# Kernel tuning notes

Measured on AMD Instinct MI355X. Metric: run time of the kernel, lower is better.

Reference implementation:

```python
import jax, jax.numpy as jnp
import numpy as np

T, H, W_, CIN, LAT, HID, OUT, NHL = 32, 64, 64, 3, 256, 256, 3, 3
OMEGA = 30.0  # SIREN sine frequency


def _uniform(key, shape, fan_in):
    b = np.sqrt(6.0 / fan_in) / OMEGA
    return jax.random.uniform(key, shape, jnp.float32, -b, b)


def setup_inputs() -> dict:
    key = jax.random.key(0)
    ks = jax.random.split(key, 10)
    return {
        "coords": jax.random.normal(ks[0], (T, H, W_, CIN), jnp.float32),
        "latents": jax.random.normal(ks[1], (T, LAT), jnp.float32),
        # shared SIREN weights (nf_net): W stored as (out, in) like nn.Linear
        "W0": _uniform(ks[2], (HID, CIN), CIN),
        "b0": jnp.zeros((HID,), jnp.float32),
        "Wh": _uniform(ks[3], (NHL, HID, HID), HID),
        "bh": jnp.zeros((NHL, HID), jnp.float32),
        "Wf": _uniform(ks[4], (OUT, HID), HID),
        "bf": jnp.zeros((OUT,), jnp.float32),
        # hypernet weight generators (hw_net), no bias
        "HW0": _uniform(ks[5], (HID * CIN, LAT), LAT),
        "HWh": _uniform(ks[6], (NHL, HID * HID, LAT), LAT),
        # hypernet bias generators (hb_net), no bias
        "HB": _uniform(ks[7], (NHL + 1, HID, LAT), LAT),
    }


def reference(coords, latents, W0, b0, Wh, bh, Wf, bf, HW0, HWh, HB):
    t = latents.shape[0]
    # per-frame hyper biases for all layers: (t, NHL+1, HID)
    hb = jnp.einsum('tl,khl->tkh', latents, HB)
    # layer 0: per-frame weight (t, HID, CIN)
    hw0 = (latents @ HW0.T).reshape(t, HID, CIN)
    x = coords  # (t,h,w,CIN)
    x = (x @ W0.T + b0
         + jnp.einsum('thwi,toi->thwo', x, hw0)
         + hb[:, 0][:, None, None, :])
    x = jnp.sin(OMEGA * x)
    for i in range(NHL):
        hw = (latents @ HWh[i].T).reshape(t, HID, HID)  # (t, HID, HID)
        x = (x @ Wh[i].T + bh[i]
             + jnp.einsum('thwi,toi->thwo', x, hw)
             + hb[:, i + 1][:, None, None, :])
        x = jnp.sin(OMEGA * x)
    return x @ Wf.T + bf  # (t,h,w,OUT)
```

## Files before the change

### kernel.cpp

```cpp
#include <hip/hip_runtime.h>
#include <cstdint>
#include <cstddef>

typedef __attribute__((ext_vector_type(8))) _Float16 f16x8;
typedef __attribute__((ext_vector_type(16))) float f32x16;

#define LO_SCALE 2048.0f
#define LO_INV   (1.0f / 2048.0f)

union H8 { f16x8 v; _Float16 h[8]; };

__global__ __launch_bounds__(256) void kab(
    const float* __restrict__ latents, const float* __restrict__ W0,
    const float* __restrict__ b0, const float* __restrict__ bh,
    const float* __restrict__ HW0, const float* __restrict__ HB,
    const float* __restrict__ Wh, const float* __restrict__ HWh,
    _Float16* __restrict__ w0blob, float* __restrict__ beff,
    _Float16* __restrict__ whblob) {
  __shared__ float lat_t[8192];
  int tid = threadIdx.x, bid = blockIdx.x;

  if (bid >= 768) {
    int id = (bid - 768) * 256 + tid;
    if (id < 32768) {
      int t = id >> 10, rem = id & 1023;
      int r2 = rem & 127, part = r2 >> 6, lane = r2 & 63;
      int nf = rem >> 7;
      int o = nf * 32 + (lane & 31), kc = lane >> 5;
      const float* lat = latents + t * 256;
      H8 outv;
#pragma unroll
      for (int j = 0; j < 8; ++j) outv.h[j] = (_Float16)0.0f;
#pragma unroll
      for (int j = 0; j < 8; ++j) {
        int i = kc * 8 + j;
        if (i < 3) {
          const float* row = HW0 + (o * 3 + i) * 256;
          float s = W0[o * 3 + i];
          for (int k = 0; k < 256; k += 4)
            s += row[k] * lat[k] + row[k + 1] * lat[k + 1] +
                 row[k + 2] * lat[k + 2] + row[k + 3] * lat[k + 3];
          _Float16 hi = (_Float16)s;
          outv.h[j] = part ? (_Float16)((s - (float)hi) * LO_SCALE) : hi;
        }
      }
      *(f16x8*)(w0blob + (size_t)id * 8) = outv.v;
    } else {
      int v = id - 32768;
      int t = v >> 10, k = (v >> 8) & 3, hm = v & 255;
      float base = (k == 0) ? b0[hm] : bh[(k - 1) * 256 + hm];
      const float* lat = latents + t * 256;
      const float* row = HB + (size_t)(k * 256 + hm) * 256;
      float s = base;
      for (int kk = 0; kk < 256; kk += 4)
        s += row[kk] * lat[kk] + row[kk + 1] * lat[kk + 1] +
             row[kk + 2] * lat[kk + 2] + row[kk + 3] * lat[kk + 3];
      beff[v] = s;
    }
    return;
  }

  int h = bid & 1, ks = (bid >> 1) & 15, nf = (bid >> 5) & 7, l = bid >> 8;

  {
    int f = tid >> 3, kb = (tid & 7) * 32;
#pragma unroll
    for (int m = 0; m < 32; m += 4) {
      float4 v = *(const float4*)(latents + f * 256 + kb + m);
      lat_t[(kb + m + 0) * 32 + f] = v.x;
      lat_t[(kb + m + 1) * 32 + f] = v.y;
      lat_t[(kb + m + 2) * 32 + f] = v.z;
      lat_t[(kb + m + 3) * 32 + f] = v.w;
    }
  }
  __syncthreads();

  int oo = tid >> 3, jj = tid & 7;
  int o = nf * 32 + oo;
  int i = ks * 16 + h * 8 + jj;
  int r = o * 256 + i;
  const float* rowp = HWh + ((size_t)l * 65536 + (size_t)r) * 256;

  float acc[32];
#pragma unroll
  for (int f = 0; f < 32; ++f) acc[f] = 0.f;

  float curf[16], nxtf[16];
#pragma unroll
  for (int q = 0; q < 4; ++q)
    *(float4*)(curf + q * 4) = *(const float4*)(rowp + q * 4);

  for (int kc = 0; kc < 16; ++kc) {
    if (kc < 15) {
#pragma unroll
      for (int q = 0; q < 4; ++q)
        *(float4*)(nxtf + q * 4) = *(const float4*)(rowp + (kc + 1) * 16 + q * 4);
    }
    const float* lp = lat_t + kc * 512;
#pragma unroll
    for (int m = 0; m < 16; ++m) {
      float hw = curf[m];
#pragma unroll
      for (int fq = 0; fq < 8; ++fq) {
        float4 lv = *(const float4*)(lp + m * 32 + fq * 4);
        acc[fq * 4 + 0] += hw * lv.x;
        acc[fq * 4 + 1] += hw * lv.y;
        acc[fq * 4 + 2] += hw * lv.z;
        acc[fq * 4 + 3] += hw * lv.w;
      }
    }
#pragma unroll
    for (int q = 0; q < 16; ++q) curf[q] = nxtf[q];
  }

  float whv = Wh[l * 65536 + r];
  size_t cbase = (size_t)(nf * 16 + ks) * 1024 + (size_t)h * 256 + (size_t)tid;
#pragma unroll
  for (int t = 0; t < 32; ++t) {
    float w = acc[t] + whv;
    _Float16 hi = (_Float16)w;
    _Float16 lo = (_Float16)((w - (float)hi) * LO_SCALE);
    size_t b = (size_t)(t * 3 + l) * 131072 + cbase;
    whblob[b] = hi;
    whblob[b + 512] = lo;
  }
}

__global__ __launch_bounds__(512, 6) void kb_siren(
    const float* __restrict__ coords, const _Float16* __restrict__ whblob,
    const _Float16* __restrict__ w0blob, const float* __restrict__ beff,
    const float* __restrict__ Wf, const float* __restrict__ bf,
    float* __restrict__ out) {
  __shared__ _Float16 xs_hi[32 * 264];
  __shared__ _Float16 xs_lo[32 * 264];
  __shared__ float wf_s[768];
  __shared__ float red[768];
  int tid = threadIdx.x;
  int bid0 = blockIdx.x;
  int bid = (bid0 & 7) * 512 + (bid0 >> 3);
  int t = bid >> 7, tile = bid & 127;
  int wv = tid >> 6, lane = tid & 63, col = lane & 31, h = lane >> 5;

  if (tid < 192) *(float4*)(wf_s + tid * 4) = *(const float4*)(Wf + tid * 4);
  if (tid < 32) {
    const float* cp = coords + (size_t)(t * 4096 + tile * 32 + tid) * 3;
    float c0 = cp[0], c1 = cp[1], c2 = cp[2];
    H8 hv, lv, z;
#pragma unroll
    for (int j = 0; j < 8; ++j) { hv.h[j] = (_Float16)0.f; lv.h[j] = (_Float16)0.f; z.h[j] = (_Float16)0.f; }
    _Float16 h0 = (_Float16)c0, h1 = (_Float16)c1, h2 = (_Float16)c2;
    hv.h[0] = h0; hv.h[1] = h1; hv.h[2] = h2;
    lv.h[0] = (_Float16)((c0 - (float)h0) * LO_SCALE);
    lv.h[1] = (_Float16)((c1 - (float)h1) * LO_SCALE);
    lv.h[2] = (_Float16)((c2 - (float)h2) * LO_SCALE);
    *(f16x8*)(xs_hi + tid * 264) = hv.v;
    *(f16x8*)(xs_lo + tid * 264) = lv.v;
    *(f16x8*)(xs_hi + tid * 264 + 8) = z.v;
    *(f16x8*)(xs_lo + tid * 264 + 8) = z.v;
  }
  __syncthreads();

  f32x16 accA, accB;

  auto init_bias = [&](int bk) {
    const float* bp = beff + ((t * 4 + bk) << 8) + wv * 32 + h * 4;
#pragma unroll
    for (int rq = 0; rq < 4; ++rq) {
      float4 bvv = *(const float4*)(bp + rq * 8);
      float ba[4];
      *(float4*)ba = bvv;
#pragma unroll
      for (int q = 0; q < 4; ++q) {
        accA[rq * 4 + q] = ba[q];
        accB[rq * 4 + q] = 0.f;
      }
    }
  };

  auto load_a = [&](const _Float16* blobL, int NS, int ks, f16x8 (&a)[2]) {
    const _Float16* p = blobL + (size_t)((wv * NS + ks) * 2) * 512 + lane * 8;
    a[0] = *(const f16x8*)p;
    a[1] = *(const f16x8*)(p + 512);
  };

  auto load_b = [&](int ks, f16x8 (&b)[2]) {
    int off = col * 264 + ks * 16 + h * 8;
    b[0] = *(const f16x8*)(xs_hi + off);
    b[1] = *(const f16x8*)(xs_lo + off);
  };

  auto mfma3 = [&](f16x8 (&a)[2], f16x8 (&b)[2]) {
    accA = __builtin_amdgcn_mfma_f32_32x32x16_f16(a[0], b[0], accA, 0, 0, 0);
    accB = __builtin_amdgcn_mfma_f32_32x32x16_f16(a[0], b[1], accB, 0, 0, 0);
    accB = __builtin_amdgcn_mfma_f32_32x32x16_f16(a[1], b[0], accB, 0, 0, 0);
  };

  auto epilogue = [&]() {
#pragma unroll
    for (int r = 0; r < 16; ++r)
      accA[r] = __sinf(30.0f * (accA[r] + accB[r] * LO_INV));
    __syncthreads();
#pragma unroll
    for (int g = 0; g < 2; ++g) {
      float seq[8];
#pragma unroll
      for (int q = 0; q < 4; ++q) {
        float oa = accA[8 * g + q];
        float ob = accA[8 * g + 4 + q];
        float send = h ? oa : ob;
        float recv = __shfl_xor(send, 32, 64);
        seq[q]     = h ? recv : oa;
        seq[4 + q] = h ? ob : recv;
      }
      H8 hv, lv;
#pragma unroll
      for (int j = 0; j < 8; ++j) {
        _Float16 hi = (_Float16)seq[j];
        hv.h[j] = hi;
        lv.h[j] = (_Float16)((seq[j] - (float)hi) * LO_SCALE);
      }
      int off = col * 264 + wv * 32 + g * 16 + h * 8;
      *(f16x8*)(xs_hi + off) = hv.v;
      *(f16x8*)(xs_lo + off) = lv.v;
    }
    __syncthreads();
  };

  init_bias(0);
  {
    f16x8 a[2], b[2];
    load_a(w0blob + (size_t)t * 8192, 1, 0, a);
    load_b(0, b);
    mfma3(a, b);
  }
  epilogue();

  for (int li = 0; li < 3; ++li) {
    init_bias(li + 1);
    const _Float16* bl = whblob + (size_t)(t * 3 + li) * 131072;
#pragma unroll
    for (int ks = 0; ks < 16; ++ks) {
      f16x8 a[2], b[2];
      load_a(bl, 16, ks, a);
      load_b(ks, b);
      mfma3(a, b);
    }
    epilogue();
  }

  {
    float pc0 = 0.f, pc1 = 0.f, pc2 = 0.f;
    int px = tid & 31, kq = tid >> 5;
#pragma unroll
    for (int cc = 0; cc < 2; ++cc) {
      int k0 = kq * 16 + cc * 8;
      H8 hv, lv;
      hv.v = *(const f16x8*)(xs_hi + px * 264 + k0);
      lv.v = *(const f16x8*)(xs_lo + px * 264 + k0);
#pragma unroll
      for (int j = 0; j < 8; ++j) {
        float xv = (float)hv.h[j] + (float)lv.h[j] * LO_INV;
        pc0 += xv * wf_s[k0 + j];
        pc1 += xv * wf_s[256 + k0 + j];
        pc2 += xv * wf_s[512 + k0 + j];
      }
    }
    pc0 += __shfl_xor(pc0, 32, 64);
    pc1 += __shfl_xor(pc1, 32, 64);
    pc2 += __shfl_xor(pc2, 32, 64);
    if (h == 0) {
      red[wv * 96 + px * 3 + 0] = pc0;
      red[wv * 96 + px * 3 + 1] = pc1;
      red[wv * 96 + px * 3 + 2] = pc2;
    }
    __syncthreads();
    if (tid < 96) {
      int p2 = tid / 3, c = tid - p2 * 3;
      float s = bf[c];
#pragma unroll
      for (int q = 0; q < 8; ++q) s += red[q * 96 + p2 * 3 + c];
      out[(size_t)(t * 4096 + tile * 32 + p2) * 3 + c] = s;
    }
  }
}

extern "C" void kernel_launch(void* const* d_in, const int* in_sizes, int n_in,
                              void* d_out, int out_size, void* d_ws, size_t ws_size,
                              hipStream_t stream) {
  const float* coords  = (const float*)d_in[0];
  const float* latents = (const float*)d_in[1];
  const float* W0      = (const float*)d_in[2];
  const float* b0      = (const float*)d_in[3];
  const float* Wh      = (const float*)d_in[4];
  const float* bh      = (const float*)d_in[5];
  const float* Wf      = (const float*)d_in[6];
  const float* bf      = (const float*)d_in[7];
  const float* HW0     = (const float*)d_in[8];
  const float* HWh     = (const float*)d_in[9];
  const float* HB      = (const float*)d_in[10];
  float* outp = (float*)d_out;

  char* w = (char*)d_ws;
  _Float16* whblob = (_Float16*)w;
  _Float16* w0blob = (_Float16*)(w + 25165824);
  float*    beff   = (float*)(w + 25690112);

  kab<<<1024, 256, 0, stream>>>(latents, W0, b0, bh, HW0, HB, Wh, HWh,
                                w0blob, beff, whblob);
  kb_siren<<<4096, 512, 0, stream>>>(coords, whblob, w0blob, beff, Wf, bf, outp);
}
```

Measured before the change: 258.7 us.

## Process 128 pixels per block to reuse weight fragments, prefetch next A

Each SIREN block now covers 128 pixels (four 32-pixel MFMA fragments) instead of 32. Every weight fragment loaded from the hypernet blob is reused across all four fragments, which cuts global and L2 weight traffic by about four times. The next k-step's weight fragment is also prefetched into registers while the current MFMAs run. In exchange, the per-block LDS tile grows to roughly 135 KB, which limits residency to about one block per CU and leaves fewer waves to hide latency; accumulator register use also grows fourfold.

```diff
diff --git a/kernel.cpp b/kernel.cpp
--- a/kernel.cpp
+++ b/kernel.cpp
@@ -126,24 +126,24 @@
   }
 }
 
-__global__ __launch_bounds__(512, 6) void kb_siren(
+__global__ __launch_bounds__(512, 2) void kb_siren(
     const float* __restrict__ coords, const _Float16* __restrict__ whblob,
     const _Float16* __restrict__ w0blob, const float* __restrict__ beff,
     const float* __restrict__ Wf, const float* __restrict__ bf,
     float* __restrict__ out) {
-  __shared__ _Float16 xs_hi[32 * 264];
-  __shared__ _Float16 xs_lo[32 * 264];
+  __shared__ _Float16 xs_hi[128 * 264];
+  __shared__ _Float16 xs_lo[128 * 264];
   __shared__ float wf_s[768];
-  __shared__ float red[768];
+  __shared__ float red[1536];
   int tid = threadIdx.x;
   int bid0 = blockIdx.x;
-  int bid = (bid0 & 7) * 512 + (bid0 >> 3);
-  int t = bid >> 7, tile = bid & 127;
+  int bid = (bid0 & 7) * 128 + (bid0 >> 3);
+  int t = bid >> 5, tile = bid & 31;
   int wv = tid >> 6, lane = tid & 63, col = lane & 31, h = lane >> 5;
 
   if (tid < 192) *(float4*)(wf_s + tid * 4) = *(const float4*)(Wf + tid * 4);
-  if (tid < 32) {
-    const float* cp = coords + (size_t)(t * 4096 + tile * 32 + tid) * 3;
+  if (tid < 128) {
+    const float* cp = coords + (size_t)(t * 4096 + tile * 128 + tid) * 3;
     float c0 = cp[0], c1 = cp[1], c2 = cp[2];
     H8 hv, lv, z;
 #pragma unroll
@@ -160,7 +160,7 @@
   }
   __syncthreads();
 
-  f32x16 accA, accB;
+  f32x16 accA[4], accB[4];
 
   auto init_bias = [&](int bk) {
     const float* bp = beff + ((t * 4 + bk) << 8) + wv * 32 + h * 4;
@@ -171,89 +171,112 @@
       *(float4*)ba = bvv;
 #pragma unroll
       for (int q = 0; q < 4; ++q) {
-        accA[rq * 4 + q] = ba[q];
-        accB[rq * 4 + q] = 0.f;
+#pragma unroll
+        for (int pf = 0; pf < 4; ++pf) {
+          accA[pf][rq * 4 + q] = ba[q];
+          accB[pf][rq * 4 + q] = 0.f;
+        }
       }
     }
   };
 
-  auto load_a = [&](const _Float16* blobL, int NS, int ks, f16x8 (&a)[2]) {
-    const _Float16* p = blobL + (size_t)((wv * NS + ks) * 2) * 512 + lane * 8;
-    a[0] = *(const f16x8*)p;
-    a[1] = *(const f16x8*)(p + 512);
+  auto aptr = [&](const _Float16* blobL, int NS, int ks) {
+    return blobL + (size_t)((wv * NS + ks) * 2) * 512 + lane * 8;
   };
 
-  auto load_b = [&](int ks, f16x8 (&b)[2]) {
-    int off = col * 264 + ks * 16 + h * 8;
-    b[0] = *(const f16x8*)(xs_hi + off);
-    b[1] = *(const f16x8*)(xs_lo + off);
+  auto mfma_ks = [&](f16x8 a0, f16x8 a1, int ks) {
+#pragma unroll
+    for (int pf = 0; pf < 4; ++pf) {
+      int off = (pf * 32 + col) * 264 + ks * 16 + h * 8;
+      f16x8 bh_ = *(const f16x8*)(xs_hi + off);
+      f16x8 bl_ = *(const f16x8*)(xs_lo + off);
+      accA[pf] = __builtin_amdgcn_mfma_f32_32x32x16_f16(a0, bh_, accA[pf], 0, 0, 0);
+      accB[pf] = __builtin_amdgcn_mfma_f32_32x32x16_f16(a0, bl_, accB[pf], 0, 0, 0);
+      accB[pf] = __builtin_amdgcn_mfma_f32_32x32x16_f16(a1, bh_, accB[pf], 0, 0, 0);
+    }
   };
 
-  auto mfma3 = [&](f16x8 (&a)[2], f16x8 (&b)[2]) {
-    accA = __builtin_amdgcn_mfma_f32_32x32x16_f16(a[0], b[0], accA, 0, 0, 0);
-    accB = __builtin_amdgcn_mfma_f32_32x32x16_f16(a[0], b[1], accB, 0, 0, 0);
-    accB = __builtin_amdgcn_mfma_f32_32x32x16_f16(a[1], b[0], accB, 0, 0, 0);
-  };
-
   auto epilogue = [&]() {
 #pragma unroll
-    for (int r = 0; r < 16; ++r)
-      accA[r] = __sinf(30.0f * (accA[r] + accB[r] * LO_INV));
+    for (int pf = 0; pf < 4; ++pf)
+#pragma unroll
+      for (int r = 0; r < 16; ++r)
+        accA[pf][r] = __sinf(30.0f * (accA[pf][r] + accB[pf][r] * LO_INV));
     __syncthreads();
 #pragma unroll
-    for (int g = 0; g < 2; ++g) {
-      float seq[8];
-#pragma unroll
-      for (int q = 0; q < 4; ++q) {
-        float oa = accA[8 * g + q];
-        float ob = accA[8 * g + 4 + q];
-        float send = h ? oa : ob;
-        float recv = __shfl_xor(send, 32, 64);
-        seq[q]     = h ? recv : oa;
-        seq[4 + q] = h ? ob : recv;
-      }
-      H8 hv, lv;
-#pragma unroll
-      for (int j = 0; j < 8; ++j) {
-        _Float16 hi = (_Float16)seq[j];
-        hv.h[j] = hi;
-        lv.h[j] = (_Float16)((seq[j] - (float)hi) * LO_SCALE);
-      }
-      int off = col * 264 + wv * 32 + g * 16 + h * 8;
-      *(f16x8*)(xs_hi + off) = hv.v;
-      *(f16x8*)(xs_lo + off) = lv.v;
-    }
+    for (int pf = 0; pf < 4; ++pf)
+#pragma unroll
+      for (int g = 0; g < 2; ++g) {
+        float seq[8];
+#pragma unroll
+        for (int q = 0; q < 4; ++q) {
+          float oa = accA[pf][8 * g + q];
+          float ob = accA[pf][8 * g + 4 + q];
+          float send = h ? oa : ob;
+          float recv = __shfl_xor(send, 32, 64);
+          seq[q]     = h ? recv : oa;
+          seq[4 + q] = h ? ob : recv;
+        }
+        H8 hv, lv;
+#pragma unroll
+        for (int j = 0; j < 8; ++j) {
+          _Float16 hi = (_Float16)seq[j];
+          hv.h[j] = hi;
+          lv.h[j] = (_Float16)((seq[j] - (float)hi) * LO_SCALE);
+        }
+        int off = (pf * 32 + col) * 264 + wv * 32 + g * 16 + h * 8;
+        *(f16x8*)(xs_hi + off) = hv.v;
+        *(f16x8*)(xs_lo + off) = lv.v;
+      }
     __syncthreads();
   };
 
+  const _Float16* bl0 = whblob + (size_t)(t * 3) * 131072;
+
   init_bias(0);
   {
-    f16x8 a[2], b[2];
-    load_a(w0blob + (size_t)t * 8192, 1, 0, a);
-    load_b(0, b);
-    mfma3(a, b);
+    const _Float16* p = aptr(w0blob + (size_t)t * 8192, 1, 0);
+    f16x8 a0 = *(const f16x8*)p, a1 = *(const f16x8*)(p + 512);
+    mfma_ks(a0, a1, 0);
+  }
+  f16x8 c0, c1;
+  {
+    const _Float16* p = aptr(bl0, 16, 0);
+    c0 = *(const f16x8*)p;
+    c1 = *(const f16x8*)(p + 512);
   }
   epilogue();
 
+#pragma unroll
   for (int li = 0; li < 3; ++li) {
     init_bias(li + 1);
     const _Float16* bl = whblob + (size_t)(t * 3 + li) * 131072;
+    const _Float16* bln = whblob + (size_t)(t * 3 + li + 1) * 131072;
 #pragma unroll
     for (int ks = 0; ks < 16; ++ks) {
-      f16x8 a[2], b[2];
-      load_a(bl, 16, ks, a);
-      load_b(ks, b);
-      mfma3(a, b);
+      f16x8 n0, n1;
+      bool have_next = (ks < 15) || (li < 2);
+      if (ks < 15) {
+        const _Float16* p = aptr(bl, 16, ks + 1);
+        n0 = *(const f16x8*)p;
+        n1 = *(const f16x8*)(p + 512);
+      } else if (li < 2) {
+        const _Float16* p = aptr(bln, 16, 0);
+        n0 = *(const f16x8*)p;
+        n1 = *(const f16x8*)(p + 512);
+      }
+      mfma_ks(c0, c1, ks);
+      if (have_next) { c0 = n0; c1 = n1; }
     }
     epilogue();
   }
 
   {
     float pc0 = 0.f, pc1 = 0.f, pc2 = 0.f;
-    int px = tid & 31, kq = tid >> 5;
-#pragma unroll
-    for (int cc = 0; cc < 2; ++cc) {
-      int k0 = kq * 16 + cc * 8;
+    int px = tid & 127, kq = tid >> 7;
+#pragma unroll
+    for (int cc = 0; cc < 8; ++cc) {
+      int k0 = kq * 64 + cc * 8;
       H8 hv, lv;
       hv.v = *(const f16x8*)(xs_hi + px * 264 + k0);
       lv.v = *(const f16x8*)(xs_lo + px * 264 + k0);
@@ -265,21 +288,16 @@
         pc2 += xv * wf_s[512 + k0 + j];
       }
     }
-    pc0 += __shfl_xor(pc0, 32, 64);
-    pc1 += __shfl_xor(pc1, 32, 64);
-    pc2 += __shfl_xor(pc2, 32, 64);
-    if (h == 0) {
-      red[wv * 96 + px * 3 + 0] = pc0;
-      red[wv * 96 + px * 3 + 1] = pc1;
-      red[wv * 96 + px * 3 + 2] = pc2;
-    }
+    red[kq * 384 + px * 3 + 0] = pc0;
+    red[kq * 384 + px * 3 + 1] = pc1;
+    red[kq * 384 + px * 3 + 2] = pc2;
     __syncthreads();
-    if (tid < 96) {
+    if (tid < 384) {
       int p2 = tid / 3, c = tid - p2 * 3;
       float s = bf[c];
 #pragma unroll
-      for (int q = 0; q < 8; ++q) s += red[q * 96 + p2 * 3 + c];
-      out[(size_t)(t * 4096 + tile * 32 + p2) * 3 + c] = s;
+      for (int q = 0; q < 4; ++q) s += red[q * 384 + p2 * 3 + c];
+      out[(size_t)(t * 4096 + tile * 128 + p2) * 3 + c] = s;
     }
   }
 }
@@ -307,5 +325,5 @@
 
   kab<<<1024, 256, 0, stream>>>(latents, W0, b0, bh, HW0, HB, Wh, HWh,
                                 w0blob, beff, whblob);
-  kb_siren<<<4096, 512, 0, stream>>>(coords, whblob, w0blob, beff, Wf, bf, outp);
+  kb_siren<<<1024, 512, 0, stream>>>(coords, whblob, w0blob, beff, Wf, bf, outp);
 }
```

Result: faster. 227.1 us (-12.2%).

## Keep SIREN activations in registers per wave, permute K layout, fold omega into weights

Applied to the files above, without the earlier changes.

The SIREN kernel now gives each wave a whole 32-pixel tile and all 256 output features. Activations stay in registers between layers, with the K ordering of the hypernet weight blobs and Wf permuted so MFMA outputs can feed the next layer's B operand directly. This removes the shared-memory activation staging, the cross-lane shuffles and the block barriers. Omega/(2π) is folded into the generated weights and biases so the sine becomes v_fract plus v_sin, and A-operand loads are double-buffered. The cost is very high register pressure at one block per CU with 256 threads, and each wave now reloads the full per-frame weights on its own.

```diff
diff --git a/kernel.cpp b/kernel.cpp
--- a/kernel.cpp
+++ b/kernel.cpp
@@ -3,12 +3,16 @@
 #include <cstddef>
 
 typedef __attribute__((ext_vector_type(8))) _Float16 f16x8;
+typedef __attribute__((ext_vector_type(2))) __fp16 h2;
 typedef __attribute__((ext_vector_type(16))) float f32x16;
 
 #define LO_SCALE 2048.0f
 #define LO_INV   (1.0f / 2048.0f)
+#define OMEGA_SC 4.774648292756860f
 
 union H8 { f16x8 v; _Float16 h[8]; };
+union HU4 { f16x8 v; h2 p[4]; _Float16 h[8]; };
+
 
 __global__ __launch_bounds__(256) void kab(
     const float* __restrict__ latents, const float* __restrict__ W0,
@@ -33,13 +37,14 @@
       for (int j = 0; j < 8; ++j) outv.h[j] = (_Float16)0.0f;
 #pragma unroll
       for (int j = 0; j < 8; ++j) {
-        int i = kc * 8 + j;
+        int i = 8 * (j >> 2) + 4 * kc + (j & 3);
         if (i < 3) {
           const float* row = HW0 + (o * 3 + i) * 256;
           float s = W0[o * 3 + i];
           for (int k = 0; k < 256; k += 4)
             s += row[k] * lat[k] + row[k + 1] * lat[k + 1] +
                  row[k + 2] * lat[k + 2] + row[k + 3] * lat[k + 3];
+          s *= OMEGA_SC;
           _Float16 hi = (_Float16)s;
           outv.h[j] = part ? (_Float16)((s - (float)hi) * LO_SCALE) : hi;
         }
@@ -55,7 +60,7 @@
       for (int kk = 0; kk < 256; kk += 4)
         s += row[kk] * lat[kk] + row[kk + 1] * lat[kk + 1] +
              row[kk + 2] * lat[kk + 2] + row[kk + 3] * lat[kk + 3];
-      beff[v] = s;
+      beff[v] = s * OMEGA_SC;
     }
     return;
   }
@@ -77,7 +82,7 @@
 
   int oo = tid >> 3, jj = tid & 7;
   int o = nf * 32 + oo;
-  int i = ks * 16 + h * 8 + jj;
+  int i = (ks >> 1) * 32 + (ks & 1) * 16 + 8 * (jj >> 2) + 4 * h + (jj & 3);
   int r = o * 256 + i;
   const float* rowp = HWh + ((size_t)l * 65536 + (size_t)r) * 256;
 
@@ -117,7 +122,7 @@
   size_t cbase = (size_t)(nf * 16 + ks) * 1024 + (size_t)h * 256 + (size_t)tid;
 #pragma unroll
   for (int t = 0; t < 32; ++t) {
-    float w = acc[t] + whv;
+    float w = (acc[t] + whv) * OMEGA_SC;
     _Float16 hi = (_Float16)w;
     _Float16 lo = (_Float16)((w - (float)hi) * LO_SCALE);
     size_t b = (size_t)(t * 3 + l) * 131072 + cbase;
@@ -126,160 +131,191 @@
   }
 }
 
-__global__ __launch_bounds__(512, 6) void kb_siren(
+__global__ __launch_bounds__(256, 1) void kb_siren(
     const float* __restrict__ coords, const _Float16* __restrict__ whblob,
     const _Float16* __restrict__ w0blob, const float* __restrict__ beff,
     const float* __restrict__ Wf, const float* __restrict__ bf,
     float* __restrict__ out) {
-  __shared__ _Float16 xs_hi[32 * 264];
-  __shared__ _Float16 xs_lo[32 * 264];
   __shared__ float wf_s[768];
-  __shared__ float red[768];
   int tid = threadIdx.x;
   int bid0 = blockIdx.x;
-  int bid = (bid0 & 7) * 512 + (bid0 >> 3);
-  int t = bid >> 7, tile = bid & 127;
+  int bid = (bid0 & 7) * 128 + (bid0 >> 3);
   int wv = tid >> 6, lane = tid & 63, col = lane & 31, h = lane >> 5;
-
-  if (tid < 192) *(float4*)(wf_s + tid * 4) = *(const float4*)(Wf + tid * 4);
-  if (tid < 32) {
-    const float* cp = coords + (size_t)(t * 4096 + tile * 32 + tid) * 3;
-    float c0 = cp[0], c1 = cp[1], c2 = cp[2];
-    H8 hv, lv, z;
-#pragma unroll
-    for (int j = 0; j < 8; ++j) { hv.h[j] = (_Float16)0.f; lv.h[j] = (_Float16)0.f; z.h[j] = (_Float16)0.f; }
-    _Float16 h0 = (_Float16)c0, h1 = (_Float16)c1, h2 = (_Float16)c2;
-    hv.h[0] = h0; hv.h[1] = h1; hv.h[2] = h2;
-    lv.h[0] = (_Float16)((c0 - (float)h0) * LO_SCALE);
-    lv.h[1] = (_Float16)((c1 - (float)h1) * LO_SCALE);
-    lv.h[2] = (_Float16)((c2 - (float)h2) * LO_SCALE);
-    *(f16x8*)(xs_hi + tid * 264) = hv.v;
-    *(f16x8*)(xs_lo + tid * 264) = lv.v;
-    *(f16x8*)(xs_hi + tid * 264 + 8) = z.v;
-    *(f16x8*)(xs_lo + tid * 264 + 8) = z.v;
+  int wave_id = bid * 4 + wv;
+  int t = wave_id >> 7, tile = wave_id & 127;
+
+  {
+    int p = tid;
+    int pn = p >> 5, pu = (p >> 4) & 1, ph = (p >> 3) & 1, pj = p & 7;
+    int orig = pn * 32 + pu * 16 + 8 * (pj >> 2) + 4 * ph + (pj & 3);
+#pragma unroll
+    for (int c = 0; c < 3; ++c)
+      wf_s[c * 256 + p] = Wf[c * 256 + orig];
   }
   __syncthreads();
 
-  f32x16 accA, accB;
-
-  auto init_bias = [&](int bk) {
-    const float* bp = beff + ((t * 4 + bk) << 8) + wv * 32 + h * 4;
+  HU4 xch[8][2], xcl[8][2], xnh[8][2], xnl[8][2];
+
+  HU4 bch, bcl;
+  {
+    const float* cp = coords + (size_t)(t * 4096 + tile * 32 + col) * 3;
+    float v0 = cp[0], v1 = cp[1], v2 = cp[2];
+    if (h) { v0 = 0.f; v1 = 0.f; v2 = 0.f; }
+#pragma unroll
+    for (int j = 0; j < 8; ++j) { bch.h[j] = (_Float16)0.f; bcl.h[j] = (_Float16)0.f; }
+    _Float16 q0 = (_Float16)v0, q1 = (_Float16)v1, q2 = (_Float16)v2;
+    bch.h[0] = q0; bch.h[1] = q1; bch.h[2] = q2;
+    bcl.h[0] = (_Float16)((v0 - (float)q0) * LO_SCALE);
+    bcl.h[1] = (_Float16)((v1 - (float)q1) * LO_SCALE);
+    bcl.h[2] = (_Float16)((v2 - (float)q2) * LO_SCALE);
+  }
+
+  auto sin2pi = [](float x) {
+    float f, r;
+    asm("v_fract_f32 %0, %1" : "=v"(f) : "v"(x));
+    asm("v_sin_f32 %0, %1" : "=v"(r) : "v"(f));
+    return r;
+  };
+
+  auto init_bias = [&](int bk, int nf, f32x16& A, f32x16& B) {
+    const float* bp = beff + ((t * 4 + bk) << 8) + nf * 32 + h * 4;
 #pragma unroll
     for (int rq = 0; rq < 4; ++rq) {
-      float4 bvv = *(const float4*)(bp + rq * 8);
+      float4 bv = *(const float4*)(bp + rq * 8);
       float ba[4];
-      *(float4*)ba = bvv;
-#pragma unroll
-      for (int q = 0; q < 4; ++q) {
-        accA[rq * 4 + q] = ba[q];
-        accB[rq * 4 + q] = 0.f;
-      }
+      *(float4*)ba = bv;
+#pragma unroll
+      for (int q = 0; q < 4; ++q) { A[rq * 4 + q] = ba[q]; B[rq * 4 + q] = 0.f; }
     }
   };
 
-  auto load_a = [&](const _Float16* blobL, int NS, int ks, f16x8 (&a)[2]) {
-    const _Float16* p = blobL + (size_t)((wv * NS + ks) * 2) * 512 + lane * 8;
-    a[0] = *(const f16x8*)p;
-    a[1] = *(const f16x8*)(p + 512);
+  auto aload = [&](const _Float16* blobL, int idx2, f16x8& ah, f16x8& al) {
+    const _Float16* p = blobL + (size_t)idx2 * 512 + lane * 8;
+    ah = *(const f16x8*)p;
+    al = *(const f16x8*)(p + 512);
   };
 
-  auto load_b = [&](int ks, f16x8 (&b)[2]) {
-    int off = col * 264 + ks * 16 + h * 8;
-    b[0] = *(const f16x8*)(xs_hi + off);
-    b[1] = *(const f16x8*)(xs_lo + off);
+  auto epi = [&](f32x16& A, f32x16& B, HU4& oh0, HU4& ol0, HU4& oh1, HU4& ol1) {
+    float val[16];
+#pragma unroll
+    for (int r = 0; r < 16; ++r) val[r] = sin2pi(fmaf(B[r], LO_INV, A[r]));
+#pragma unroll
+    for (int k = 0; k < 4; ++k) {
+      h2 hp = __builtin_amdgcn_cvt_pkrtz(val[2 * k], val[2 * k + 1]);
+      oh0.p[k] = hp;
+      ol0.p[k] = __builtin_amdgcn_cvt_pkrtz((val[2 * k] - (float)hp[0]) * LO_SCALE,
+                                            (val[2 * k + 1] - (float)hp[1]) * LO_SCALE);
+      h2 hq = __builtin_amdgcn_cvt_pkrtz(val[8 + 2 * k], val[8 + 2 * k + 1]);
+      oh1.p[k] = hq;
+      ol1.p[k] = __builtin_amdgcn_cvt_pkrtz((val[8 + 2 * k] - (float)hq[0]) * LO_SCALE,
+                                            (val[8 + 2 * k + 1] - (float)hq[1]) * LO_SCALE);
+    }
   };
 
-  auto mfma3 = [&](f16x8 (&a)[2], f16x8 (&b)[2]) {
-    accA = __builtin_amdgcn_mfma_f32_32x32x16_f16(a[0], b[0], accA, 0, 0, 0);
-    accB = __builtin_amdgcn_mfma_f32_32x32x16_f16(a[0], b[1], accB, 0, 0, 0);
-    accB = __builtin_amdgcn_mfma_f32_32x32x16_f16(a[1], b[0], accB, 0, 0, 0);
-  };
-
-  auto epilogue = [&]() {
-#pragma unroll
-    for (int r = 0; r < 16; ++r)
-      accA[r] = __sinf(30.0f * (accA[r] + accB[r] * LO_INV));
-    __syncthreads();
-#pragma unroll
-    for (int g = 0; g < 2; ++g) {
-      float seq[8];
-#pragma unroll
-      for (int q = 0; q < 4; ++q) {
-        float oa = accA[8 * g + q];
-        float ob = accA[8 * g + 4 + q];
-        float send = h ? oa : ob;
-        float recv = __shfl_xor(send, 32, 64);
-        seq[q]     = h ? recv : oa;
-        seq[4 + q] = h ? ob : recv;
-      }
-      H8 hv, lv;
-#pragma unroll
-      for (int j = 0; j < 8; ++j) {
-        _Float16 hi = (_Float16)seq[j];
-        hv.h[j] = hi;
-        lv.h[j] = (_Float16)((seq[j] - (float)hi) * LO_SCALE);
-      }
-      int off = col * 264 + wv * 32 + g * 16 + h * 8;
-      *(f16x8*)(xs_hi + off) = hv.v;
-      *(f16x8*)(xs_lo + off) = lv.v;
-    }
-    __syncthreads();
-  };
-
-  init_bias(0);
-  {
-    f16x8 a[2], b[2];
-    load_a(w0blob + (size_t)t * 8192, 1, 0, a);
-    load_b(0, b);
-    mfma3(a, b);
-  }
-  epilogue();
-
+  {
+    const _Float16* w0b = w0blob + (size_t)t * 8192;
+    f16x8 Ph[2][2], Pl[2][2];
+    aload(w0b, 0, Ph[0][0], Pl[0][0]);
+    aload(w0b, 2, Ph[0][1], Pl[0][1]);
+    aload(w0b, 4, Ph[1][0], Pl[1][0]);
+    aload(w0b, 6, Ph[1][1], Pl[1][1]);
+#pragma unroll
+    for (int np = 0; np < 4; ++np) {
+      int par = np & 1;
+      f32x16 aA0, aB0, aA1, aB1;
+      init_bias(0, np * 2, aA0, aB0);
+      init_bias(0, np * 2 + 1, aA1, aB1);
+      f16x8 a0h = Ph[par][0], a0l = Pl[par][0];
+      f16x8 a1h = Ph[par][1], a1l = Pl[par][1];
+      if (np + 2 < 4) {
+        aload(w0b, (np * 2 + 4) * 2, Ph[par][0], Pl[par][0]);
+        aload(w0b, (np * 2 + 5) * 2, Ph[par][1], Pl[par][1]);
+      }
+      aA0 = __builtin_amdgcn_mfma_f32_32x32x16_f16(a0h, bch.v, aA0, 0, 0, 0);
+      aA1 = __builtin_amdgcn_mfma_f32_32x32x16_f16(a1h, bch.v, aA1, 0, 0, 0);
+      aB0 = __builtin_amdgcn_mfma_f32_32x32x16_f16(a0h, bcl.v, aB0, 0, 0, 0);
+      aB1 = __builtin_amdgcn_mfma_f32_32x32x16_f16(a1h, bcl.v, aB1, 0, 0, 0);
+      aB0 = __builtin_amdgcn_mfma_f32_32x32x16_f16(a0l, bch.v, aB0, 0, 0, 0);
+      aB1 = __builtin_amdgcn_mfma_f32_32x32x16_f16(a1l, bch.v, aB1, 0, 0, 0);
+      epi(aA0, aB0, xch[np * 2][0], xcl[np * 2][0], xch[np * 2][1], xcl[np * 2][1]);
+      epi(aA1, aB1, xch[np * 2 + 1][0], xcl[np * 2 + 1][0], xch[np * 2 + 1][1], xcl[np * 2 + 1][1]);
+    }
+  }
+
+#pragma unroll 1
   for (int li = 0; li < 3; ++li) {
-    init_bias(li + 1);
     const _Float16* bl = whblob + (size_t)(t * 3 + li) * 131072;
 #pragma unroll
-    for (int ks = 0; ks < 16; ++ks) {
-      f16x8 a[2], b[2];
-      load_a(bl, 16, ks, a);
-      load_b(ks, b);
-      mfma3(a, b);
-    }
-    epilogue();
+    for (int np = 0; np < 4; ++np) {
+      int f0 = np * 2, f1 = np * 2 + 1;
+      f32x16 aA0, aB0, aA1, aB1;
+      init_bias(li + 1, f0, aA0, aB0);
+      init_bias(li + 1, f1, aA1, aB1);
+      f16x8 S0h[2], S0l[2], S1h[2], S1l[2];
+      aload(bl, (f0 * 16 + 0) * 2, S0h[0], S0l[0]);
+      aload(bl, (f1 * 16 + 0) * 2, S1h[0], S1l[0]);
+      aload(bl, (f0 * 16 + 1) * 2, S0h[1], S0l[1]);
+      aload(bl, (f1 * 16 + 1) * 2, S1h[1], S1l[1]);
+#pragma unroll
+      for (int ks = 0; ks < 16; ++ks) {
+        f16x8 a0h = S0h[ks & 1], a0l = S0l[ks & 1];
+        f16x8 a1h = S1h[ks & 1], a1l = S1l[ks & 1];
+        if (ks + 2 < 16) {
+          aload(bl, (f0 * 16 + ks + 2) * 2, S0h[ks & 1], S0l[ks & 1]);
+          aload(bl, (f1 * 16 + ks + 2) * 2, S1h[ks & 1], S1l[ks & 1]);
+        }
+        int q = ks >> 1, s = ks & 1;
+        f16x8 bh_ = xch[q][s].v;
+        f16x8 bl_ = xcl[q][s].v;
+        aA0 = __builtin_amdgcn_mfma_f32_32x32x16_f16(a0h, bh_, aA0, 0, 0, 0);
+        aA1 = __builtin_amdgcn_mfma_f32_32x32x16_f16(a1h, bh_, aA1, 0, 0, 0);
+        aB0 = __builtin_amdgcn_mfma_f32_32x32x16_f16(a0h, bl_, aB0, 0, 0, 0);
+        aB1 = __builtin_amdgcn_mfma_f32_32x32x16_f16(a1h, bl_, aB1, 0, 0, 0);
+        aB0 = __builtin_amdgcn_mfma_f32_32x32x16_f16(a0l, bh_, aB0, 0, 0, 0);
+        aB1 = __builtin_amdgcn_mfma_f32_32x32x16_f16(a1l, bh_, aB1, 0, 0, 0);
+      }
+      epi(aA0, aB0, xnh[f0][0], xnl[f0][0], xnh[f0][1], xnl[f0][1]);
+      epi(aA1, aB1, xnh[f1][0], xnl[f1][0], xnh[f1][1], xnl[f1][1]);
+    }
+#pragma unroll
+    for (int i2 = 0; i2 < 8; ++i2)
+#pragma unroll
+      for (int s2 = 0; s2 < 2; ++s2) {
+        xch[i2][s2].v = xnh[i2][s2].v;
+        xcl[i2][s2].v = xnl[i2][s2].v;
+      }
   }
 
   {
     float pc0 = 0.f, pc1 = 0.f, pc2 = 0.f;
-    int px = tid & 31, kq = tid >> 5;
-#pragma unroll
-    for (int cc = 0; cc < 2; ++cc) {
-      int k0 = kq * 16 + cc * 8;
-      H8 hv, lv;
-      hv.v = *(const f16x8*)(xs_hi + px * 264 + k0);
-      lv.v = *(const f16x8*)(xs_lo + px * 264 + k0);
-#pragma unroll
-      for (int j = 0; j < 8; ++j) {
-        float xv = (float)hv.h[j] + (float)lv.h[j] * LO_INV;
-        pc0 += xv * wf_s[k0 + j];
-        pc1 += xv * wf_s[256 + k0 + j];
-        pc2 += xv * wf_s[512 + k0 + j];
-      }
-    }
+#pragma unroll
+    for (int nf = 0; nf < 8; ++nf)
+#pragma unroll
+      for (int s = 0; s < 2; ++s) {
+        const float* wp = wf_s + nf * 32 + s * 16 + h * 8;
+        float w0a[8], w1a[8], w2a[8];
+        *(float4*)(w0a) = *(const float4*)(wp);
+        *(float4*)(w0a + 4) = *(const float4*)(wp + 4);
+        *(float4*)(w1a) = *(const float4*)(wp + 256);
+        *(float4*)(w1a + 4) = *(const float4*)(wp + 260);
+        *(float4*)(w2a) = *(const float4*)(wp + 512);
+        *(float4*)(w2a + 4) = *(const float4*)(wp + 516);
+#pragma unroll
+        for (int j = 0; j < 8; ++j) {
+          float xv = (float)xch[nf][s].h[j] + (float)xcl[nf][s].h[j] * LO_INV;
+          pc0 += xv * w0a[j];
+          pc1 += xv * w1a[j];
+          pc2 += xv * w2a[j];
+        }
+      }
     pc0 += __shfl_xor(pc0, 32, 64);
     pc1 += __shfl_xor(pc1, 32, 64);
     pc2 += __shfl_xor(pc2, 32, 64);
     if (h == 0) {
-      red[wv * 96 + px * 3 + 0] = pc0;
-      red[wv * 96 + px * 3 + 1] = pc1;
-      red[wv * 96 + px * 3 + 2] = pc2;
-    }
-    __syncthreads();
-    if (tid < 96) {
-      int p2 = tid / 3, c = tid - p2 * 3;
-      float s = bf[c];
-#pragma unroll
-      for (int q = 0; q < 8; ++q) s += red[q * 96 + p2 * 3 + c];
-      out[(size_t)(t * 4096 + tile * 32 + p2) * 3 + c] = s;
+      size_t o = (size_t)(t * 4096 + tile * 32 + col) * 3;
+      out[o + 0] = pc0 + bf[0];
+      out[o + 1] = pc1 + bf[1];
+      out[o + 2] = pc2 + bf[2];
     }
   }
 }
@@ -307,5 +343,5 @@
 
   kab<<<1024, 256, 0, stream>>>(latents, W0, b0, bh, HW0, HB, Wh, HWh,
                                 w0blob, beff, whblob);
-  kb_siren<<<4096, 512, 0, stream>>>(coords, whblob, w0blob, beff, Wf, bf, outp);
+  kb_siren<<<1024, 256, 0, stream>>>(coords, whblob, w0blob, beff, Wf, bf, outp);
 }
```

New measurement: 341.9 us. 1.32x slower.
